# Kernel tuning notes

Measured on AMD Instinct MI355X. Metric: run time of the kernel, lower is better.

Reference implementation:

```python
import jax, jax.numpy as jnp
import numpy as np

L = 128          # bandlimit (max_l)
NTHETA = 256     # Gauss-Legendre latitudes (>= L for exact quadrature)
NPHI = 512       # longitudes (>= 2L-1)
C_IN, C_OUT = 32, 32


def _normalized_assoc_legendre(Lmax, xg):
    """Pbar_lm(x) with Condon-Shortley phase, orthonormal on the sphere.
    Returns (Lmax, Lmax, T) for m>=0; zero for m>l."""
    T = xg.shape[0]
    P = np.zeros((Lmax, Lmax, T), dtype=np.float64)
    sx = np.sqrt(np.maximum(1.0 - xg * xg, 0.0))
    P[0, 0] = 1.0 / np.sqrt(4.0 * np.pi)
    for m in range(1, Lmax):
        P[m, m] = -np.sqrt((2 * m + 1) / (2.0 * m)) * sx * P[m - 1, m - 1]
    for m in range(0, Lmax - 1):
        P[m + 1, m] = np.sqrt(2 * m + 3.0) * xg * P[m, m]
    for m in range(Lmax):
        for l in range(m + 2, Lmax):
            a = np.sqrt((4.0 * l * l - 1.0) / (l * l - m * m))
            b = np.sqrt(((l - 1.0) ** 2 - m * m) / (4.0 * (l - 1.0) ** 2 - 1.0))
            P[l, m] = a * (xg * P[l - 1, m] - b * P[l - 2, m])
    return P


def _build_basis():
    # Gauss-Legendre quadrature in cos(theta): exact for degree <= 2*NTHETA-1
    xg, wg = np.polynomial.legendre.leggauss(NTHETA)
    P = _normalized_assoc_legendre(L, xg)  # (L, L, T), m>=0
    # Full basis B[l, m+L-1, t]; Pbar_{l,-m} = (-1)^m Pbar_{l,m}
    B = np.zeros((L, 2 * L - 1, NTHETA), dtype=np.float64)
    for m in range(-(L - 1), L):
        B[:, m + L - 1, :] = ((-1.0) ** abs(m) if m < 0 else 1.0) * P[:, abs(m), :]
    return B.astype(np.float32), wg.astype(np.float32)


def setup_inputs() -> dict:
    key = jax.random.key(0)
    k1, k2, k3 = jax.random.split(key, 3)
    x = jax.random.normal(k1, (NTHETA, NPHI, C_IN), dtype=jnp.float32)
    std = 1.0 / (C_IN + C_OUT)
    wr = std * jax.random.normal(k2, (L, 2 * L - 1, C_IN, C_OUT), dtype=jnp.float32)
    wi = std * jax.random.normal(k3, (L, 2 * L - 1, C_IN, C_OUT), dtype=jnp.float32)
    B, wg = _build_basis()
    return {"x": x, "weights_real": wr, "weights_imag": wi,
            "legendre": jnp.asarray(B), "quad_w": jnp.asarray(wg)}


def reference(x, weights_real, weights_imag, legendre, quad_w):
    ntheta, nphi, _ = x.shape
    Lb = legendre.shape[0]
    # --- forward SHT (per channel, vectorized) ---
    # longitude FFT: Fm[t,k,c] = sum_p x e^{-i 2pi k p / nphi}; dphi = 2pi/nphi
    Fm = jnp.fft.fft(x.astype(jnp.complex64), axis=1) * (2.0 * np.pi / nphi)
    midx = np.arange(-(Lb - 1), Lb) % nphi            # FFT bins for m=-(L-1)..L-1
    Fm_sel = Fm[:, midx, :]                           # (t, 2L-1, c)
    Bw = legendre * quad_w[None, None, :]             # quadrature-weighted basis
    # flm[l,m,c] = sum_t w_t Pbar_lm(theta_t) Fm[t,m,c]
    flm = jnp.einsum('lmt,tmc->lmc', Bw.astype(jnp.complex64), Fm_sel)
    # --- spectral conv: per-(l,m) channel mixing ---
    W = weights_real.astype(jnp.complex64) + 1j * weights_imag.astype(jnp.complex64)
    y = jnp.einsum('lmc,lmco->lmo', flm, W)           # (L, 2L-1, O)
    # --- inverse SHT ---
    G = jnp.einsum('lmt,lmo->tmo', legendre.astype(jnp.complex64), y)  # (t, 2L-1, O)
    spec = jnp.zeros((ntheta, nphi, G.shape[-1]), dtype=jnp.complex64)
    spec = spec.at[:, midx, :].set(G)
    out = jnp.fft.ifft(spec, axis=1) * nphi           # f = sum_m G e^{i m phi}
    return jnp.moveaxis(out.real, 2, 0)               # (O, ntheta, nphi)
```

## Files before the change

kernel.cpp:

```cpp
#include <hip/hip_runtime.h>
#include <math.h>

#define DEVFN __global__ __launch_bounds__(256)
#define DEVFN4 __global__ __launch_bounds__(256, 4)

namespace {
constexpr int LL  = 128;
constexpr int MM2 = 255;
constexpr int NT  = 256;
constexpr int NP  = 512;
constexpr int NC  = 32;
constexpr int NO  = 32;
constexpr float TWO_PI = 6.283185307179586476925286766559f;
}

typedef short v8s __attribute__((ext_vector_type(8)));
typedef float v4f __attribute__((ext_vector_type(4)));

__device__ inline unsigned short f2bf(float f) {
  unsigned int u = __float_as_uint(f);
  return (unsigned short)((u + 0x7FFFu + ((u >> 16) & 1u)) >> 16);
}

DEVFN void kp_prep(const float* __restrict__ x, unsigned short* __restrict__ tw1t,
                   unsigned short* __restrict__ vt, unsigned short* __restrict__ xb) {
  __shared__ float sm[32][65];
  const int bid = blockIdx.x;
  const int tid = threadIdx.x;
  const float phi = TWO_PI / (float)NP;
  if (bid < 512) {
    const int idx = bid * 256 + tid;
    const float fs = TWO_PI / (float)NP;
    {
      const int n = idx >> 9, p = idx & 511;
      const int m = n >> 1;
      const int k = (m * p) & (NP - 1);
      float s, c;
      sincosf(phi * (float)k, &s, &c);
      tw1t[idx] = f2bf((n & 1) ? (-s * fs) : (c * fs));
    }
    {
      const int p = idx >> 8, k = idx & 255;
      const int m = k >> 1;
      const int kk = (m * p) & (NP - 1);
      float s, c;
      sincosf(phi * (float)kk, &s, &c);
      vt[idx] = f2bf((k & 1) ? s : c);
    }
  } else {
    const int q = bid - 512;
    const int t = q >> 3;
    const int p0 = (q & 7) * 64;
#pragma unroll
    for (int i = 0; i < 8; ++i) {
      const int idx = tid + i * 256;
      const int p = idx >> 5, c = idx & 31;
      sm[c][p] = x[((size_t)t * NP + p0 + p) * NC + c];
    }
    __syncthreads();
    const int c = tid >> 3, pg = tid & 7;
    unsigned short pk[8];
#pragma unroll
    for (int u = 0; u < 8; ++u) pk[u] = f2bf(sm[c][pg * 8 + u]);
    *(uint4*)(xb + ((size_t)(t * 32 + c)) * NP + p0 + pg * 8) = *(const uint4*)pk;
  }
}

DEVFN void k1_mfma(const unsigned short* __restrict__ xb,
                   const unsigned short* __restrict__ tw1t,
                   const float* __restrict__ wg,
                   float* __restrict__ fwr, float* __restrict__ fwi) {
  __shared__ unsigned short As[128 * 32];
  __shared__ unsigned short Bs[64 * 32];
  const int tid = threadIdx.x;
  const int r0 = blockIdx.x * 128;
  const int n0 = blockIdx.y * 64;
  const int wid = tid >> 6, lane = tid & 63;
  const int wm = wid & 1, wn = wid >> 1;
  v4f acc[4][2];
#pragma unroll
  for (int i = 0; i < 4; ++i)
#pragma unroll
    for (int j = 0; j < 2; ++j) {
      acc[i][j][0] = 0.f; acc[i][j][1] = 0.f; acc[i][j][2] = 0.f; acc[i][j][3] = 0.f;
    }
  const int lr = lane & 15, lk = (lane >> 4) * 8;
  for (int k0 = 0; k0 < 512; k0 += 32) {
#pragma unroll
    for (int s = 0; s < 3; ++s) {
      const int chunk = tid + s * 256;
      if (chunk < 512) {
        const int row = chunk >> 2, c16 = chunk & 3;
        *(uint4*)&As[row * 32 + c16 * 8] =
            *(const uint4*)&xb[(size_t)(r0 + row) * 512 + k0 + c16 * 8];
      } else {
        const int bc = chunk - 512;
        const int row = bc >> 2, c16 = bc & 3;
        *(uint4*)&Bs[row * 32 + c16 * 8] =
            *(const uint4*)&tw1t[(size_t)(n0 + row) * 512 + k0 + c16 * 8];
      }
    }
    __syncthreads();
    v8s af[4], bf[2];
#pragma unroll
    for (int i = 0; i < 4; ++i) af[i] = *(const v8s*)&As[(wm * 64 + i * 16 + lr) * 32 + lk];
#pragma unroll
    for (int j = 0; j < 2; ++j) bf[j] = *(const v8s*)&Bs[(wn * 32 + j * 16 + lr) * 32 + lk];
#pragma unroll
    for (int i = 0; i < 4; ++i)
#pragma unroll
      for (int j = 0; j < 2; ++j)
        acc[i][j] = __builtin_amdgcn_mfma_f32_16x16x32_bf16(af[i], bf[j], acc[i][j], 0, 0, 0);
    __syncthreads();
  }
  const int lrow = (lane >> 4) * 4;
#pragma unroll
  for (int i = 0; i < 4; ++i) {
    const int rbase = r0 + wm * 64 + i * 16 + lrow;
    const int t = rbase >> 5, c0 = rbase & 31;
    const float w = wg[t];
#pragma unroll
    for (int j = 0; j < 2; ++j) {
      const int n = n0 + wn * 32 + j * 16 + lr;
      const int mI = n >> 1;
      float* dst = (n & 1) ? fwi : fwr;
      float4 v = {acc[i][j][0] * w, acc[i][j][1] * w, acc[i][j][2] * w, acc[i][j][3] * w};
      *(float4*)&dst[((size_t)mI * NT + t) * NC + c0] = v;
    }
  }
}

DEVFN4 void k2_flm(const float* __restrict__ leg, const float* __restrict__ fwr,
                   const float* __restrict__ fwi, float* __restrict__ flr,
                   float* __restrict__ fli) {
  const int m = blockIdx.x;
  const int wid = threadIdx.x >> 6, lane = threadIdx.x & 63;
  const int lb = m + blockIdx.y * 16 + wid * 4;
  if (lb >= LL) return;
  const int c = lane & 31;
  const float* fp = ((lane >> 5) ? fwi : fwr) + (size_t)m * NT * NC + c;
  const float* lg[4];
#pragma unroll
  for (int i = 0; i < 4; ++i) {
    const int l = min(lb + i, LL - 1);
    lg[i] = leg + ((size_t)(l * MM2 + 127 + m)) * NT;
  }
  float a[4] = {};
#pragma unroll 2
  for (int t = 0; t < NT; t += 4) {
    const float f0 = fp[(t + 0) * NC];
    const float f1 = fp[(t + 1) * NC];
    const float f2 = fp[(t + 2) * NC];
    const float f3 = fp[(t + 3) * NC];
#pragma unroll
    for (int i = 0; i < 4; ++i) {
      const float4 b = *(const float4*)(lg[i] + t);
      a[i] = fmaf(b.x, f0, a[i]);
      a[i] = fmaf(b.y, f1, a[i]);
      a[i] = fmaf(b.z, f2, a[i]);
      a[i] = fmaf(b.w, f3, a[i]);
    }
  }
  float* outp = (lane >> 5) ? fli : flr;
#pragma unroll
  for (int i = 0; i < 4; ++i)
    if (lb + i < LL) outp[(size_t)(m * LL + lb + i) * NC + c] = a[i];
}

DEVFN4 void k3_mix(const float* __restrict__ flr, const float* __restrict__ fli,
                   const float* __restrict__ wr, const float* __restrict__ wi,
                   float* __restrict__ ya, float* __restrict__ yb) {
  const int m = blockIdx.x;
  const int wid = threadIdx.x >> 6, lane = threadIdx.x & 63;
  const int l = m + blockIdx.y * 4 + wid;
  if (l >= LL) return;
  const int c8 = lane >> 3;
  const int o8 = lane & 7;
  const int c0 = c8 * 4, o0 = o8 * 4;
  const float s0 = (m > 0) ? 1.0f : 0.0f;
  const size_t rp = ((size_t)(l * MM2 + 127 + m) * NC) * NO;
  const size_t rn = ((size_t)(l * MM2 + 127 - m) * NC) * NO;
  float4 Wrp[4], Wrn[4], Wip[4], Win[4];
#pragma unroll
  for (int i = 0; i < 4; ++i) {
    const size_t co = (size_t)(c0 + i) * NO + o0;
    Wrp[i] = *(const float4*)&wr[rp + co];
    Wrn[i] = *(const float4*)&wr[rn + co];
    Wip[i] = *(const float4*)&wi[rp + co];
    Win[i] = *(const float4*)&wi[rn + co];
  }
  const float4 fa4 = *(const float4*)&flr[(size_t)(m * LL + l) * NC + c0];
  const float4 fb4 = *(const float4*)&fli[(size_t)(m * LL + l) * NC + c0];
  float4 accA = {0.f, 0.f, 0.f, 0.f}, accB = {0.f, 0.f, 0.f, 0.f};
#pragma unroll
  for (int i = 0; i < 4; ++i) {
    const float fa = (i == 0) ? fa4.x : (i == 1) ? fa4.y : (i == 2) ? fa4.z : fa4.w;
    const float fb = (i == 0) ? fb4.x : (i == 1) ? fb4.y : (i == 2) ? fb4.z : fb4.w;
    float4 wa, wb;
    wa.x = fmaf(s0, Wrn[i].x, Wrp[i].x); wa.y = fmaf(s0, Wrn[i].y, Wrp[i].y);
    wa.z = fmaf(s0, Wrn[i].z, Wrp[i].z); wa.w = fmaf(s0, Wrn[i].w, Wrp[i].w);
    wb.x = fmaf(s0, Win[i].x, -Wip[i].x); wb.y = fmaf(s0, Win[i].y, -Wip[i].y);
    wb.z = fmaf(s0, Win[i].z, -Wip[i].z); wb.w = fmaf(s0, Win[i].w, -Wip[i].w);
    accA.x = fmaf(fa, wa.x, fmaf(fb, wb.x, accA.x));
    accA.y = fmaf(fa, wa.y, fmaf(fb, wb.y, accA.y));
    accA.z = fmaf(fa, wa.z, fmaf(fb, wb.z, accA.z));
    accA.w = fmaf(fa, wa.w, fmaf(fb, wb.w, accA.w));
    accB.x = fmaf(fa, wb.x, fmaf(-fb, wa.x, accB.x));
    accB.y = fmaf(fa, wb.y, fmaf(-fb, wa.y, accB.y));
    accB.z = fmaf(fa, wb.z, fmaf(-fb, wa.z, accB.z));
    accB.w = fmaf(fa, wb.w, fmaf(-fb, wa.w, accB.w));
  }
#pragma unroll
  for (int mask = 8; mask <= 32; mask <<= 1) {
    accA.x += __shfl_xor(accA.x, mask); accA.y += __shfl_xor(accA.y, mask);
    accA.z += __shfl_xor(accA.z, mask); accA.w += __shfl_xor(accA.w, mask);
    accB.x += __shfl_xor(accB.x, mask); accB.y += __shfl_xor(accB.y, mask);
    accB.z += __shfl_xor(accB.z, mask); accB.w += __shfl_xor(accB.w, mask);
  }
  if (c8 == 0) {
    *(float4*)&ya[(size_t)(m * LL + l) * NO + o0] = accA;
    *(float4*)&yb[(size_t)(m * LL + l) * NO + o0] = accB;
  }
}

DEVFN4 void k4_G(const float* __restrict__ leg, const float* __restrict__ ya,
                 const float* __restrict__ yb, unsigned short* __restrict__ ut) {
  const int m = blockIdx.x;
  const int tc = blockIdx.y;
  const int o = threadIdx.x & 31;
  const int tq = threadIdx.x >> 5;
  const int t0 = tc * 32 + tq * 4;
  float aa[4] = {}, bb[4] = {};
#pragma unroll 8
  for (int l = m; l < LL; ++l) {
    const float4 g = *(const float4*)(leg + ((size_t)(l * MM2 + 127 + m)) * NT + t0);
    const float yav = ya[(m * LL + l) * NO + o];
    const float ybv = yb[(m * LL + l) * NO + o];
    aa[0] = fmaf(g.x, yav, aa[0]);  bb[0] = fmaf(g.x, ybv, bb[0]);
    aa[1] = fmaf(g.y, yav, aa[1]);  bb[1] = fmaf(g.y, ybv, bb[1]);
    aa[2] = fmaf(g.z, yav, aa[2]);  bb[2] = fmaf(g.z, ybv, bb[2]);
    aa[3] = fmaf(g.w, yav, aa[3]);  bb[3] = fmaf(g.w, ybv, bb[3]);
  }
#pragma unroll
  for (int i = 0; i < 4; ++i) {
    const unsigned int pk = (unsigned int)f2bf(aa[i]) | ((unsigned int)f2bf(bb[i]) << 16);
    *(unsigned int*)&ut[((size_t)((t0 + i) * 32 + o)) * 256 + 2 * m] = pk;
  }
}

DEVFN void k5_mfma(const unsigned short* __restrict__ ut,
                   const unsigned short* __restrict__ vt,
                   float* __restrict__ out) {
  __shared__ unsigned short As[128 * 32];
  __shared__ unsigned short Bs[128 * 32];
  const int tid = threadIdx.x;
  const int p0 = blockIdx.x * 128;
  const int r0 = blockIdx.y * 128;
  const int wid = tid >> 6, lane = tid & 63;
  const int wm = wid & 1, wn = wid >> 1;
  v4f acc[4][4];
#pragma unroll
  for (int i = 0; i < 4; ++i)
#pragma unroll
    for (int j = 0; j < 4; ++j) {
      acc[i][j][0] = 0.f; acc[i][j][1] = 0.f; acc[i][j][2] = 0.f; acc[i][j][3] = 0.f;
    }
  const int lr = lane & 15, lk = (lane >> 4) * 8;
  for (int k0 = 0; k0 < 256; k0 += 32) {
#pragma unroll
    for (int s = 0; s < 2; ++s) {
      const int chunk = tid + s * 256;
      const int row = chunk >> 2, c16 = chunk & 3;
      *(uint4*)&As[row * 32 + c16 * 8] =
          *(const uint4*)&vt[(size_t)(p0 + row) * 256 + k0 + c16 * 8];
      *(uint4*)&Bs[row * 32 + c16 * 8] =
          *(const uint4*)&ut[(size_t)(r0 + row) * 256 + k0 + c16 * 8];
    }
    __syncthreads();
    v8s af[4], bf[4];
#pragma unroll
    for (int i = 0; i < 4; ++i) af[i] = *(const v8s*)&As[(wm * 64 + i * 16 + lr) * 32 + lk];
#pragma unroll
    for (int j = 0; j < 4; ++j) bf[j] = *(const v8s*)&Bs[(wn * 64 + j * 16 + lr) * 32 + lk];
#pragma unroll
    for (int i = 0; i < 4; ++i)
#pragma unroll
      for (int j = 0; j < 4; ++j)
        acc[i][j] = __builtin_amdgcn_mfma_f32_16x16x32_bf16(af[i], bf[j], acc[i][j], 0, 0, 0);
    __syncthreads();
  }
  const int lrow = (lane >> 4) * 4;
#pragma unroll
  for (int i = 0; i < 4; ++i) {
    const int pbase = p0 + wm * 64 + i * 16 + lrow;
#pragma unroll
    for (int j = 0; j < 4; ++j) {
      const int r = r0 + wn * 64 + j * 16 + lr;
      const int t = r >> 5, o = r & 31;
      float4 v = {acc[i][j][0], acc[i][j][1], acc[i][j][2], acc[i][j][3]};
      *(float4*)&out[((size_t)o * NT + t) * NP + pbase] = v;
    }
  }
}

extern "C" void kernel_launch(void* const* d_in, const int* in_sizes, int n_in,
                              void* d_out, int out_size, void* d_ws, size_t ws_size,
                              hipStream_t stream) {
  const float* x   = (const float*)d_in[0];
  const float* wr  = (const float*)d_in[1];
  const float* wi  = (const float*)d_in[2];
  const float* leg = (const float*)d_in[3];
  const float* wg  = (const float*)d_in[4];
  float* out = (float*)d_out;

  unsigned short* tw1t = (unsigned short*)d_ws;
  unsigned short* vt   = tw1t + 131072;
  unsigned short* xb   = vt + 131072;
  unsigned short* ut   = xb + 4194304;
  float* fwr = (float*)(ut + 2097152);
  float* fwi = fwr + 1048576;
  float* flr = fwi + 1048576;
  float* fli = flr + 524288;
  float* ya  = fli + 524288;
  float* yb  = ya + 524288;

  hipLaunchKernelGGL(kp_prep, dim3(2560), dim3(256), 0, stream, x, tw1t, vt, xb);
  hipLaunchKernelGGL(k1_mfma, dim3(64, 4), dim3(256), 0, stream, xb, tw1t, wg, fwr, fwi);
  hipLaunchKernelGGL(k2_flm, dim3(128, 8), dim3(256), 0, stream, leg, fwr, fwi, flr, fli);
  hipLaunchKernelGGL(k3_mix, dim3(128, 32), dim3(256), 0, stream, flr, fli, wr, wi, ya, yb);
  hipLaunchKernelGGL(k4_G, dim3(128, 8), dim3(256), 0, stream, leg, ya, yb, ut);
  hipLaunchKernelGGL(k5_mfma, dim3(4, 64), dim3(256), 0, stream, ut, vt, out);
}
```

Before: 381.2 us.

## Split Legendre reductions across waves and l-chunks to raise parallelism

```diff
diff --git a/kernel.cpp b/kernel.cpp
--- a/kernel.cpp
+++ b/kernel.cpp
@@ -2,7 +2,6 @@
 #include <math.h>
 
 #define DEVFN __global__ __launch_bounds__(256)
-#define DEVFN4 __global__ __launch_bounds__(256, 4)
 
 namespace {
 constexpr int LL  = 128;
@@ -130,13 +129,14 @@
   }
 }
 
-DEVFN4 void k2_flm(const float* __restrict__ leg, const float* __restrict__ fwr,
-                   const float* __restrict__ fwi, float* __restrict__ flr,
-                   float* __restrict__ fli) {
+DEVFN void k2_flm(const float* __restrict__ leg, const float* __restrict__ fwr,
+                  const float* __restrict__ fwi, float* __restrict__ flr,
+                  float* __restrict__ fli) {
+  __shared__ float sp[4][4][64];
   const int m = blockIdx.x;
+  const int lb = m + blockIdx.y * 4;
+  if (lb >= LL) return;
   const int wid = threadIdx.x >> 6, lane = threadIdx.x & 63;
-  const int lb = m + blockIdx.y * 16 + wid * 4;
-  if (lb >= LL) return;
   const int c = lane & 31;
   const float* fp = ((lane >> 5) ? fwi : fwr) + (size_t)m * NT * NC + c;
   const float* lg[4];
@@ -146,8 +146,10 @@
     lg[i] = leg + ((size_t)(l * MM2 + 127 + m)) * NT;
   }
   float a[4] = {};
+  const int tbeg = wid * 64;
 #pragma unroll 2
-  for (int t = 0; t < NT; t += 4) {
+  for (int tt = 0; tt < 64; tt += 4) {
+    const int t = tbeg + tt;
     const float f0 = fp[(t + 0) * NC];
     const float f1 = fp[(t + 1) * NC];
     const float f2 = fp[(t + 2) * NC];
@@ -161,16 +163,22 @@
       a[i] = fmaf(b.w, f3, a[i]);
     }
   }
-  float* outp = (lane >> 5) ? fli : flr;
-#pragma unroll
-  for (int i = 0; i < 4; ++i)
-    if (lb + i < LL) outp[(size_t)(m * LL + lb + i) * NC + c] = a[i];
-}
-
-DEVFN4 void k3_mix(const float* __restrict__ flr, const float* __restrict__ fli,
-                   const float* __restrict__ wr, const float* __restrict__ wi,
-                   float* __restrict__ ya, float* __restrict__ yb) {
-  const int m = blockIdx.x;
+#pragma unroll
+  for (int i = 0; i < 4; ++i) sp[wid][i][lane] = a[i];
+  __syncthreads();
+  const int l = lb + wid;
+  if (l < LL) {
+    const float tot = ((sp[0][wid][lane] + sp[1][wid][lane]) +
+                       sp[2][wid][lane]) + sp[3][wid][lane];
+    float* outp = (lane >> 5) ? fli : flr;
+    outp[(size_t)(m * LL + l) * NC + c] = tot;
+  }
+}
+
+DEVFN void k3_mix(const float* __restrict__ flr, const float* __restrict__ fli,
+                  const float* __restrict__ wr, const float* __restrict__ wi,
+                  float* __restrict__ ya, float* __restrict__ yb) {
+  const int m  = blockIdx.x;
   const int wid = threadIdx.x >> 6, lane = threadIdx.x & 63;
   const int l = m + blockIdx.y * 4 + wid;
   if (l >= LL) return;
@@ -180,27 +188,23 @@
   const float s0 = (m > 0) ? 1.0f : 0.0f;
   const size_t rp = ((size_t)(l * MM2 + 127 + m) * NC) * NO;
   const size_t rn = ((size_t)(l * MM2 + 127 - m) * NC) * NO;
-  float4 Wrp[4], Wrn[4], Wip[4], Win[4];
-#pragma unroll
-  for (int i = 0; i < 4; ++i) {
-    const size_t co = (size_t)(c0 + i) * NO + o0;
-    Wrp[i] = *(const float4*)&wr[rp + co];
-    Wrn[i] = *(const float4*)&wr[rn + co];
-    Wip[i] = *(const float4*)&wi[rp + co];
-    Win[i] = *(const float4*)&wi[rn + co];
-  }
   const float4 fa4 = *(const float4*)&flr[(size_t)(m * LL + l) * NC + c0];
   const float4 fb4 = *(const float4*)&fli[(size_t)(m * LL + l) * NC + c0];
   float4 accA = {0.f, 0.f, 0.f, 0.f}, accB = {0.f, 0.f, 0.f, 0.f};
 #pragma unroll
   for (int i = 0; i < 4; ++i) {
+    const int c = c0 + i;
+    const float4 wrp = *(const float4*)&wr[rp + (size_t)c * NO + o0];
+    const float4 wrn = *(const float4*)&wr[rn + (size_t)c * NO + o0];
+    const float4 wip = *(const float4*)&wi[rp + (size_t)c * NO + o0];
+    const float4 win = *(const float4*)&wi[rn + (size_t)c * NO + o0];
     const float fa = (i == 0) ? fa4.x : (i == 1) ? fa4.y : (i == 2) ? fa4.z : fa4.w;
     const float fb = (i == 0) ? fb4.x : (i == 1) ? fb4.y : (i == 2) ? fb4.z : fb4.w;
     float4 wa, wb;
-    wa.x = fmaf(s0, Wrn[i].x, Wrp[i].x); wa.y = fmaf(s0, Wrn[i].y, Wrp[i].y);
-    wa.z = fmaf(s0, Wrn[i].z, Wrp[i].z); wa.w = fmaf(s0, Wrn[i].w, Wrp[i].w);
-    wb.x = fmaf(s0, Win[i].x, -Wip[i].x); wb.y = fmaf(s0, Win[i].y, -Wip[i].y);
-    wb.z = fmaf(s0, Win[i].z, -Wip[i].z); wb.w = fmaf(s0, Win[i].w, -Wip[i].w);
+    wa.x = fmaf(s0, wrn.x, wrp.x); wa.y = fmaf(s0, wrn.y, wrp.y);
+    wa.z = fmaf(s0, wrn.z, wrp.z); wa.w = fmaf(s0, wrn.w, wrp.w);
+    wb.x = fmaf(s0, win.x, -wip.x); wb.y = fmaf(s0, win.y, -wip.y);
+    wb.z = fmaf(s0, win.z, -wip.z); wb.w = fmaf(s0, win.w, -wip.w);
     accA.x = fmaf(fa, wa.x, fmaf(fb, wb.x, accA.x));
     accA.y = fmaf(fa, wa.y, fmaf(fb, wb.y, accA.y));
     accA.z = fmaf(fa, wa.z, fmaf(fb, wb.z, accA.z));
@@ -223,16 +227,18 @@
   }
 }
 
-DEVFN4 void k4_G(const float* __restrict__ leg, const float* __restrict__ ya,
-                 const float* __restrict__ yb, unsigned short* __restrict__ ut) {
-  const int m = blockIdx.x;
-  const int tc = blockIdx.y;
-  const int o = threadIdx.x & 31;
+DEVFN void k4_G(const float* __restrict__ leg, const float* __restrict__ ya,
+                const float* __restrict__ yb, float* __restrict__ gp) {
+  const int m  = blockIdx.x;
+  const int tc = blockIdx.y & 7;
+  const int lq = blockIdx.y >> 3;
+  const int o  = threadIdx.x & 31;
   const int tq = threadIdx.x >> 5;
   const int t0 = tc * 32 + tq * 4;
+  const int lstart = max(m, lq * 32);
+  const int lend   = (lq + 1) * 32;
   float aa[4] = {}, bb[4] = {};
-#pragma unroll 8
-  for (int l = m; l < LL; ++l) {
+  for (int l = lstart; l < lend; ++l) {
     const float4 g = *(const float4*)(leg + ((size_t)(l * MM2 + 127 + m)) * NT + t0);
     const float yav = ya[(m * LL + l) * NO + o];
     const float ybv = yb[(m * LL + l) * NO + o];
@@ -241,14 +247,16 @@
     aa[2] = fmaf(g.z, yav, aa[2]);  bb[2] = fmaf(g.z, ybv, bb[2]);
     aa[3] = fmaf(g.w, yav, aa[3]);  bb[3] = fmaf(g.w, ybv, bb[3]);
   }
-#pragma unroll
-  for (int i = 0; i < 4; ++i) {
-    const unsigned int pk = (unsigned int)f2bf(aa[i]) | ((unsigned int)f2bf(bb[i]) << 16);
-    *(unsigned int*)&ut[((size_t)((t0 + i) * 32 + o)) * 256 + 2 * m] = pk;
-  }
-}
-
-DEVFN void k5_mfma(const unsigned short* __restrict__ ut,
+  float* gq = gp + (size_t)lq * (256 * 8192);
+#pragma unroll
+  for (int i = 0; i < 4; ++i) {
+    const size_t rr = (size_t)(t0 + i) * 32 + o;
+    gq[(size_t)(2 * m) * 8192 + rr] = aa[i];
+    gq[(size_t)(2 * m + 1) * 8192 + rr] = bb[i];
+  }
+}
+
+DEVFN void k5_mfma(const float* __restrict__ gp,
                    const unsigned short* __restrict__ vt,
                    float* __restrict__ out) {
   __shared__ unsigned short As[128 * 32];
@@ -266,6 +274,8 @@
       acc[i][j][0] = 0.f; acc[i][j][1] = 0.f; acc[i][j][2] = 0.f; acc[i][j][3] = 0.f;
     }
   const int lr = lane & 15, lk = (lane >> 4) * 8;
+  const int ke = tid >> 3, rq = tid & 7;
+  constexpr size_t Q = (size_t)256 * 8192;
   for (int k0 = 0; k0 < 256; k0 += 32) {
 #pragma unroll
     for (int s = 0; s < 2; ++s) {
@@ -273,8 +283,23 @@
       const int row = chunk >> 2, c16 = chunk & 3;
       *(uint4*)&As[row * 32 + c16 * 8] =
           *(const uint4*)&vt[(size_t)(p0 + row) * 256 + k0 + c16 * 8];
-      *(uint4*)&Bs[row * 32 + c16 * 8] =
-          *(const uint4*)&ut[(size_t)(r0 + row) * 256 + k0 + c16 * 8];
+    }
+#pragma unroll
+    for (int j4 = 0; j4 < 4; ++j4) {
+      const size_t base = (size_t)(k0 + ke) * 8192 + r0 + rq * 16 + j4 * 4;
+      float4 s0 = *(const float4*)&gp[base];
+      const float4 a1 = *(const float4*)&gp[base + Q];
+      const float4 a2 = *(const float4*)&gp[base + 2 * Q];
+      const float4 a3 = *(const float4*)&gp[base + 3 * Q];
+      s0.x = ((s0.x + a1.x) + a2.x) + a3.x;
+      s0.y = ((s0.y + a1.y) + a2.y) + a3.y;
+      s0.z = ((s0.z + a1.z) + a2.z) + a3.z;
+      s0.w = ((s0.w + a1.w) + a2.w) + a3.w;
+      const int rbase = rq * 16 + j4 * 4;
+      Bs[(rbase + 0) * 32 + ke] = f2bf(s0.x);
+      Bs[(rbase + 1) * 32 + ke] = f2bf(s0.y);
+      Bs[(rbase + 2) * 32 + ke] = f2bf(s0.z);
+      Bs[(rbase + 3) * 32 + ke] = f2bf(s0.w);
     }
     __syncthreads();
     v8s af[4], bf[4];
@@ -316,18 +341,18 @@
   unsigned short* tw1t = (unsigned short*)d_ws;
   unsigned short* vt   = tw1t + 131072;
   unsigned short* xb   = vt + 131072;
-  unsigned short* ut   = xb + 4194304;
-  float* fwr = (float*)(ut + 2097152);
+  float* fwr = (float*)(xb + 4194304);
   float* fwi = fwr + 1048576;
   float* flr = fwi + 1048576;
   float* fli = flr + 524288;
   float* ya  = fli + 524288;
   float* yb  = ya + 524288;
+  float* gp  = yb + 524288;
 
   hipLaunchKernelGGL(kp_prep, dim3(2560), dim3(256), 0, stream, x, tw1t, vt, xb);
   hipLaunchKernelGGL(k1_mfma, dim3(64, 4), dim3(256), 0, stream, xb, tw1t, wg, fwr, fwi);
-  hipLaunchKernelGGL(k2_flm, dim3(128, 8), dim3(256), 0, stream, leg, fwr, fwi, flr, fli);
+  hipLaunchKernelGGL(k2_flm, dim3(128, 32), dim3(256), 0, stream, leg, fwr, fwi, flr, fli);
   hipLaunchKernelGGL(k3_mix, dim3(128, 32), dim3(256), 0, stream, flr, fli, wr, wi, ya, yb);
-  hipLaunchKernelGGL(k4_G, dim3(128, 8), dim3(256), 0, stream, leg, ya, yb, ut);
-  hipLaunchKernelGGL(k5_mfma, dim3(4, 64), dim3(256), 0, stream, ut, vt, out);
-}
+  hipLaunchKernelGGL(k4_G, dim3(128, 32), dim3(256), 0, stream, leg, ya, yb, gp);
+  hipLaunchKernelGGL(k5_mfma, dim3(4, 64), dim3(256), 0, stream, gp, vt, out);
+}
```

New measurement: 380.4 us. Within noise of the previous version (-0.2%).
